# Kernel tuning notes

Measured on AMD Instinct MI355X. Metric: run time of the kernel, lower is better.

Reference implementation:

```python
import jax, jax.numpy as jnp
import numpy as np

N_HEADS = 8
N_POINTS = 4
EPS = 1e-5


def _conv1x1(x, w, b):
    # x: [B,C,H,W], w: [O,C]
    return jnp.einsum('bchw,oc->bohw', x, w) + b[None, :, None, None]


def _gn(x, g, b, groups=32):
    B, C, H, W = x.shape
    xr = x.reshape(B, groups, C // groups, H, W)
    m = xr.mean((2, 3, 4), keepdims=True)
    v = xr.var((2, 3, 4), keepdims=True)
    xn = ((xr - m) * jax.lax.rsqrt(v + EPS)).reshape(B, C, H, W)
    return xn * g[None, :, None, None] + b[None, :, None, None]


def _ln(x, g, b):
    m = x.mean(-1, keepdims=True)
    v = x.var(-1, keepdims=True)
    return (x - m) * jax.lax.rsqrt(v + EPS) * g + b


def _ln_spec(x, g2, b2, n):
    # modality-specific LayerNorm: separate params for v tokens [:n] and i tokens [n:]
    return jnp.concatenate([_ln(x[:, :n], g2[0], b2[0]), _ln(x[:, n:], g2[1], b2[1])], 1)


def _sine_pos(h, w, d):
    nf = d // 2
    scale = 2.0 * np.pi
    ye = jnp.arange(1, h + 1, dtype=jnp.float32) / h * scale
    xe = jnp.arange(1, w + 1, dtype=jnp.float32) / w * scale
    dim_t = 10000.0 ** (2.0 * (jnp.arange(nf) // 2).astype(jnp.float32) / nf)
    def enc(e):
        p = e[:, None] / dim_t
        return jnp.stack([jnp.sin(p[:, 0::2]), jnp.cos(p[:, 1::2])], -1).reshape(e.shape[0], nf)
    py = enc(ye)  # [h,nf]
    px = enc(xe)  # [w,nf]
    pos = jnp.concatenate([jnp.broadcast_to(py[:, None, :], (h, w, nf)),
                           jnp.broadcast_to(px[None, :, :], (h, w, nf))], -1)
    return pos.reshape(h * w, d)


def _bilinear(vl, loc):
    # vl: [B,h,w,Hd,Dh] value for one level, loc: [B,Lq,Hd,P,2] normalized (x,y)
    B, h, w, Hd, Dh = vl.shape
    Lq, P = loc.shape[1], loc.shape[3]
    x = loc[..., 0] * w - 0.5
    y = loc[..., 1] * h - 0.5
    x0 = jnp.floor(x)
    y0 = jnp.floor(y)
    wx = x - x0
    wy = y - y0
    x0i = x0.astype(jnp.int32)
    y0i = y0.astype(jnp.int32)
    v2 = vl.reshape(B, h * w, Hd, Dh).transpose(0, 2, 1, 3)  # [B,Hd,HW,Dh]
    def g(ix, iy):
        valid = ((ix >= 0) & (ix < w) & (iy >= 0) & (iy < h)).astype(vl.dtype)
        flat = jnp.clip(iy, 0, h - 1) * w + jnp.clip(ix, 0, w - 1)  # [B,Lq,Hd,P]
        idx = flat.transpose(0, 2, 1, 3).reshape(B, Hd, Lq * P)
        gv = jnp.take_along_axis(v2, idx[..., None], axis=2)  # [B,Hd,Lq*P,Dh]
        gv = gv.reshape(B, Hd, Lq, P, Dh).transpose(0, 2, 1, 3, 4)  # [B,Lq,Hd,P,Dh]
        return gv * valid[..., None]
    return (g(x0i, y0i) * ((1 - wx) * (1 - wy))[..., None]
            + g(x0i + 1, y0i) * (wx * (1 - wy))[..., None]
            + g(x0i, y0i + 1) * ((1 - wx) * wy)[..., None]
            + g(x0i + 1, y0i + 1) * (wx * wy)[..., None])


def _deform_attn(q, src, ref, shapes, ow, ob, aww, awb, vw, vb, opw, opb):
    B, Len, D = src.shape
    L = len(shapes)
    Hd, P = N_HEADS, N_POINTS
    Dh = D // Hd
    value = src @ vw + vb
    off = (q @ ow + ob).reshape(B, Len, Hd, L, P, 2)
    aw = jax.nn.softmax((q @ aww + awb).reshape(B, Len, Hd, L * P), -1).reshape(B, Len, Hd, L, P)
    norm = jnp.array([[s[1], s[0]] for s in shapes], jnp.float32)  # (w,h) per level
    loc = ref[None, :, None, None, None, :] + off / norm[None, None, None, :, None, :]
    out = jnp.zeros((B, Len, Hd, Dh), value.dtype)
    start = 0
    for l, (hh, ww) in enumerate(shapes):
        vl = value[:, start:start + hh * ww].reshape(B, hh, ww, Hd, Dh)
        samp = _bilinear(vl, loc[:, :, :, l])  # [B,Len,Hd,P,Dh]
        out = out + (samp * aw[:, :, :, l, :, None]).sum(3)
        start += hh * ww
    return out.reshape(B, Len, D) @ opw + opb


def _forward(input_v, input_i, av_w, av_b, av_g, av_be, ai_w, ai_b, ai_g, ai_be,
             level_embed, off_w, off_b, aw_w, aw_b, vp_w, vp_b, op_w, op_b,
             ln1_g, ln1_b, ffn1_w, ffn1_b, ffn2_w, ffn2_b, ln2_g, ln2_b,
             as_w, as_b, as_g, as_be):
    b, c, h, w = input_v.shape
    D = av_w.shape[0]
    hw = h * w
    fv = _gn(_conv1x1(input_v, av_w, av_b), av_g, av_be)
    fi = _gn(_conv1x1(input_i, ai_w, ai_b), ai_g, ai_be)
    sv = fv.reshape(b, D, hw).transpose(0, 2, 1)
    si = fi.reshape(b, D, hw).transpose(0, 2, 1)
    src = jnp.concatenate([sv, si], 1)  # [b, 2hw, D]
    pos = _sine_pos(h, w, D)
    posf = jnp.concatenate([pos + level_embed[0], pos + level_embed[1]], 0)
    gx = (jnp.arange(w, dtype=jnp.float32) + 0.5) / w
    gy = (jnp.arange(h, dtype=jnp.float32) + 0.5) / h
    X, Y = jnp.meshgrid(gx, gy)
    ref1 = jnp.stack([X, Y], -1).reshape(hw, 2)
    ref = jnp.concatenate([ref1, ref1], 0)  # [2hw, 2]
    shapes = [(h, w), (h, w)]
    for i in range(off_w.shape[0]):
        q = src + posf
        attn = _deform_attn(q, src, ref, shapes, off_w[i], off_b[i], aw_w[i], aw_b[i],
                            vp_w[i], vp_b[i], op_w[i], op_b[i])
        src = _ln_spec(src + attn, ln1_g[i], ln1_b[i], hw)
        ff = jax.nn.relu(src @ ffn1_w[i] + ffn1_b[i]) @ ffn2_w[i] + ffn2_b[i]
        src = _ln_spec(src + ff, ln2_g[i], ln2_b[i], hw)
    out = src[:, :hw] + src[:, hw:]  # chunk along tokens, sum modalities
    out = out.transpose(0, 2, 1).reshape(b, D, h, w)
    return _gn(_conv1x1(out, as_w, as_b), as_g, as_be)


def setup_inputs():
    key = jax.random.key(0)
    B, C, H, W = 16, 768, 20, 20
    D, NL, Hd, L, P, Dff = 512, 6, N_HEADS, 2, N_POINTS, 1024
    ks = iter(jax.random.split(key, 64))
    def rn(shape, scale=0.02):
        return jax.random.normal(next(ks), shape, jnp.float32) * scale
    return {
        'input_v': jax.random.normal(next(ks), (B, C, H, W), jnp.float32),
        'input_i': jax.random.normal(next(ks), (B, C, H, W), jnp.float32),
        'av_w': rn((D, C)), 'av_b': jnp.zeros((D,)), 'av_g': jnp.ones((D,)), 'av_be': jnp.zeros((D,)),
        'ai_w': rn((D, C)), 'ai_b': jnp.zeros((D,)), 'ai_g': jnp.ones((D,)), 'ai_be': jnp.zeros((D,)),
        'level_embed': rn((L, D)),
        'off_w': rn((NL, D, Hd * L * P * 2)), 'off_b': rn((NL, Hd * L * P * 2), 0.5),
        'aw_w': rn((NL, D, Hd * L * P)), 'aw_b': jnp.zeros((NL, Hd * L * P)),
        'vp_w': rn((NL, D, D)), 'vp_b': jnp.zeros((NL, D)),
        'op_w': rn((NL, D, D)), 'op_b': jnp.zeros((NL, D)),
        'ln1_g': jnp.ones((NL, 2, D)), 'ln1_b': jnp.zeros((NL, 2, D)),
        'ffn1_w': rn((NL, D, Dff)), 'ffn1_b': jnp.zeros((NL, Dff)),
        'ffn2_w': rn((NL, Dff, D)), 'ffn2_b': jnp.zeros((NL, D)),
        'ln2_g': jnp.ones((NL, 2, D)), 'ln2_b': jnp.zeros((NL, 2, D)),
        'as_w': rn((C, D)), 'as_b': jnp.zeros((C,)), 'as_g': jnp.ones((C,)), 'as_be': jnp.zeros((C,)),
    }


def reference(input_v, input_i, av_w, av_b, av_g, av_be, ai_w, ai_b, ai_g, ai_be,
              level_embed, off_w, off_b, aw_w, aw_b, vp_w, vp_b, op_w, op_b,
              ln1_g, ln1_b, ffn1_w, ffn1_b, ffn2_w, ffn2_b, ln2_g, ln2_b,
              as_w, as_b, as_g, as_be):
    return _forward(input_v, input_i, av_w, av_b, av_g, av_be, ai_w, ai_b, ai_g, ai_be,
                    level_embed, off_w, off_b, aw_w, aw_b, vp_w, vp_b, op_w, op_b,
                    ln1_g, ln1_b, ffn1_w, ffn1_b, ffn2_w, ffn2_b, ln2_g, ln2_b,
                    as_w, as_b, as_g, as_be)
```

## Files before the change

### kernel.cpp

```cpp
#include <hip/hip_runtime.h>
#include <hip/hip_bf16.h>
#include <cstddef>
#include <math.h>


constexpr int kB   = 16;
constexpr int kCin = 768;
constexpr int kHW  = 400;
constexpr int kWpx = 20;
constexpr int kHpx = 20;
constexpr int kD   = 512;
constexpr int kLen = 800;
constexpr int kDff = 1024;
constexpr int kNL  = 6;
constexpr float kEps = 1e-5f;

typedef __attribute__((ext_vector_type(8))) short s8v;
typedef __attribute__((ext_vector_type(4))) short s4v;
typedef __attribute__((ext_vector_type(4))) float f4v;

__device__ __forceinline__ int swzk(int row, int k) {
  return (k & ~31) | ((((k >> 3) + (row >> 1)) & 3) << 3) | (k & 7);
}

__device__ __forceinline__ unsigned short f2b(float f) {
  union { __hip_bfloat16 h; unsigned short u; } cv;
  cv.h = __float2bfloat16(f);
  return cv.u;
}

__device__ __forceinline__ float b2f(unsigned short u) {
  return __uint_as_float(((unsigned)u) << 16);
}

__device__ __forceinline__ void gll(const unsigned short* g, unsigned short* l) {
  __builtin_amdgcn_global_load_lds(
      (const __attribute__((address_space(1))) unsigned int*)g,
      (__attribute__((address_space(3))) unsigned int*)l, 16, 0, 0);
}

__device__ __forceinline__ void breduce2(float& s, float& s2, float* sh) {
#pragma unroll
  for (int o = 32; o > 0; o >>= 1) {
    s  += __shfl_down(s, o);
    s2 += __shfl_down(s2, o);
  }
  const int wid = threadIdx.x >> 6, lane = threadIdx.x & 63;
  if (lane == 0) { sh[wid] = s; sh[4 + wid] = s2; }
  __syncthreads();
  if (threadIdx.x == 0) {
    sh[0] = sh[0] + sh[1] + sh[2] + sh[3];
    sh[4] = sh[4] + sh[5] + sh[6] + sh[7];
  }
  __syncthreads();
  s = sh[0]; s2 = sh[4];
}

template<int EPI>
__global__ __launch_bounds__(256)
void mgemm(const unsigned short* __restrict__ Abf,
           const unsigned short* __restrict__ Bw,
           const float* __restrict__ bias,
           const unsigned short* __restrict__ resb,
           float* __restrict__ Cf, float* __restrict__ Cf2,
           const float* __restrict__ aux,
           unsigned short* __restrict__ Cb,
           int K, int ldc, int Nreal)
{
  __shared__ unsigned short As[2][4096];
  __shared__ unsigned short Bs[2][4096];
  const int tid = threadIdx.x;
  const int w = tid >> 6, l = tid & 63;
  const int m0 = blockIdx.y * 128;
  const int n0 = blockIdx.x * 128;

  f4v acc[4][4] = {};

  const int srow = w * 32 + (l >> 2);
  const unsigned short* ga0 = Abf + (size_t)(m0 + srow) * K + (l & 3) * 8;
  const unsigned short* ga1 = ga0 + (size_t)16 * K;
  const unsigned short* gb0 = Bw + (size_t)(n0 + srow) * K + (l & 3) * 8;
  const unsigned short* gb1 = gb0 + (size_t)16 * K;
  const int lb0 = (w * 32) * 32;
  const int lb1 = (w * 32 + 16) * 32;

  int aoff[4], boff[4];
#pragma unroll
  for (int f = 0; f < 4; f++) {
    const int ra = (w >> 1) * 64 + f * 16 + (l & 15);
    aoff[f] = ra * 32 + ((((l >> 4) + (ra >> 1)) & 3) << 3);
    const int rb = (w & 1) * 64 + f * 16 + (l & 15);
    boff[f] = rb * 32 + ((((l >> 4) + (rb >> 1)) & 3) << 3);
  }

  const int NT = K >> 5;
  gll(ga0, &As[0][lb0]); gll(ga1, &As[0][lb1]);
  gll(gb0, &Bs[0][lb0]); gll(gb1, &Bs[0][lb1]);
  __syncthreads();

  for (int t = 0; t < NT; ++t) {
    const int cur = t & 1;
    if (t + 1 < NT) {
      const int ko = (t + 1) * 32;
      const int nb = cur ^ 1;
      gll(ga0 + ko, &As[nb][lb0]); gll(ga1 + ko, &As[nb][lb1]);
      gll(gb0 + ko, &Bs[nb][lb0]); gll(gb1 + ko, &Bs[nb][lb1]);
    }
    s8v af[4], bf4[4];
#pragma unroll
    for (int f = 0; f < 4; f++) {
      af[f]  = *(const s8v*)&As[cur][aoff[f]];
      bf4[f] = *(const s8v*)&Bs[cur][boff[f]];
    }
#pragma unroll
    for (int i = 0; i < 4; i++)
#pragma unroll
      for (int j = 0; j < 4; j++)
        acc[i][j] = __builtin_amdgcn_mfma_f32_16x16x32_bf16(af[i], bf4[j], acc[i][j], 0, 0, 0);
    __syncthreads();
  }

  const int colb = n0 + (w & 1) * 64;
  const int rowb = m0 + (w >> 1) * 64 + (l >> 4) * 4;
#pragma unroll
  for (int i = 0; i < 4; i++) {
#pragma unroll
    for (int j = 0; j < 4; j++) {
      const int col = colb + j * 16 + (l & 15);
      float bv;
      if (EPI == 4) bv = (col < kD) ? bias[col] : 0.0f;
      else          bv = bias[col];
#pragma unroll
      for (int r = 0; r < 4; r++) {
        const int row = rowb + i * 16 + r;
        float v = acc[i][j][r] + bv;
        if (EPI == 0) {
          Cf[(size_t)row * ldc + col] = v;
        } else if (EPI == 1) {
          Cb[(size_t)row * ldc + swzk(row, col)] = f2b(fmaxf(v, 0.0f));
        } else if (EPI == 2) {
          v += b2f(resb[(size_t)row * kD + swzk(row, col)]);
          Cb[(size_t)row * kD + col] = f2b(v);
        } else if (EPI == 3) {
          const int bb = row / kHW, p = row % kHW;
          Cf[((size_t)bb * Nreal + col) * kHW + p] = v;
        } else if (EPI == 4) {
          if (col < kD) {
            Cb[(size_t)row * kD + col] = f2b(v);
          } else {
            const int c = col - kD;
            if (c < 192)
              Cf2[(size_t)row * 192 + c] = v + aux[(size_t)(row % kLen) * 192 + c];
          }
        } else {
          if (row < kLen) {
            const int ll = col >> 8, c = col & 255;
            if (c < 192)
              Cf[(((size_t)ll * kLen) + row) * 192 + c] = v;
          }
        }
      }
    }
  }
}

__device__ __forceinline__ void cvt8t(const float* __restrict__ W,
                                      unsigned short* __restrict__ out,
                                      int K, int N, int g)
{
  const int n = g % N;
  const int k = (g / N) * 8;
  s8v p;
#pragma unroll
  for (int j = 0; j < 8; j++) p[j] = (short)f2b(W[(size_t)(k + j) * N + n]);
  const int base = n * K + (k & ~31) + ((((k >> 3) + (n >> 1)) & 3) << 3);
  *(s8v*)&out[base] = p;
}

__global__ __launch_bounds__(256)
void cvt_all_k(const float* __restrict__ vp_w, const float* __restrict__ op_w,
               const float* __restrict__ off_w, const float* __restrict__ aw_w,
               const float* __restrict__ f1w_a, const float* __restrict__ f2w_a,
               unsigned short* __restrict__ wall)
{
  const int lyr = blockIdx.x / 832;
  int g = (blockIdx.x % 832) * 256 + threadIdx.x;
  unsigned short* wl = wall + (size_t)lyr * 1703936;
  if (g < 32768) { cvt8t(vp_w + (size_t)lyr * kD * kD, wl, 512, 512, g); return; }
  g -= 32768;
  if (g < 16384) {
    const int n = g & 255;
    const int k = (g >> 8) * 8;
    const float* ow  = off_w + (size_t)lyr * kD * 128;
    const float* aww = aw_w  + (size_t)lyr * kD * 64;
    s8v p;
#pragma unroll
    for (int j = 0; j < 8; j++) {
      float v = 0.0f;
      if (n < 128)      v = ow[(size_t)(k + j) * 128 + n];
      else if (n < 192) v = aww[(size_t)(k + j) * 64 + (n - 128)];
      p[j] = (short)f2b(v);
    }
    const int row = 512 + n;
    const int base = row * 512 + (k & ~31) + ((((k >> 3) + (row >> 1)) & 3) << 3);
    *(s8v*)&wl[base] = p;
    return;
  }
  g -= 16384;
  if (g < 32768) { cvt8t(op_w + (size_t)lyr * kD * kD, wl + 393216, 512, 512, g); return; }
  g -= 32768;
  if (g < 65536) { cvt8t(f1w_a + (size_t)lyr * kD * kDff, wl + 655360, 512, 1024, g); return; }
  g -= 65536;
  cvt8t(f2w_a + (size_t)lyr * kDff * kD, wl + 1179648, 1024, 512, g);
}

__global__ __launch_bounds__(256)
void cvt_pre_k(const float* __restrict__ off_w, const float* __restrict__ aw_w,
               const float* __restrict__ off_b, const float* __restrict__ aw_b,
               unsigned short* __restrict__ woaw_all, float* __restrict__ biasall)
{
  int g = blockIdx.x * 256 + threadIdx.x;
  if (g < 98304) {
    const int l = g >> 14;
    const int gg = g & 16383;
    const int n = gg & 255;
    const int k = (gg >> 8) * 8;
    const float* ow = off_w + (size_t)l * kD * 128;
    const float* aww = aw_w + (size_t)l * kD * 64;
    s8v p;
#pragma unroll
    for (int j = 0; j < 8; j++) {
      float v = 0.0f;
      if (n < 128)      v = ow[(size_t)(k + j) * 128 + n];
      else if (n < 192) v = aww[(size_t)(k + j) * 64 + (n - 128)];
      p[j] = (short)f2b(v);
    }
    const int row = l * 256 + n;
    const int base = row * 512 + (k & ~31) + ((((k >> 3) + (row >> 1)) & 3) << 3);
    *(s8v*)&woaw_all[base] = p;
    return;
  }
  g -= 98304;
  const int l = g >> 8, c = g & 255;
  float v = 0.0f;
  if (c < 128)      v = off_b[l * 128 + c];
  else if (c < 192) v = aw_b[l * 64 + (c - 128)];
  biasall[l * 256 + c] = v;
}

__global__ void cvtw_d_k(const float* __restrict__ W, unsigned short* __restrict__ out,
                         int K, int N)
{
  const int gid = blockIdx.x * 256 + threadIdx.x;
  const int K8 = K >> 3;
  const int n  = gid / K8;
  const int k  = (gid % K8) * 8;
  s8v p;
#pragma unroll
  for (int j = 0; j < 8; j++) p[j] = (short)f2b(W[(size_t)n * K + k + j]);
  const int base = n * K + (k & ~31) + ((((k >> 3) + (n >> 1)) & 3) << 3);
  *(s8v*)&out[base] = p;
}

__global__ void tin_k(const float* __restrict__ in, unsigned short* __restrict__ out)
{
  __shared__ float t[16][17];
  const int b = blockIdx.z, c0 = blockIdx.x * 16, p0 = blockIdx.y * 16;
  const int tx = threadIdx.x & 15, ty = threadIdx.x >> 4;
  t[ty][tx] = in[((size_t)b * kCin + c0 + ty) * kHW + p0 + tx];
  __syncthreads();
  const int row = b * kHW + p0 + ty;
  const int c = c0 + tx;
  out[(size_t)row * kCin + swzk(row, c)] = f2b(t[tx][ty]);
}

__global__ void posfb_k(unsigned short* __restrict__ posfb,
                        const float* __restrict__ level_embed)
{
  const int gid = blockIdx.x * 256 + threadIdx.x;
  const int d0 = (gid & 63) * 8;
  const int t  = gid >> 6;
  s8v o;
  if (t >= kLen) {
#pragma unroll
    for (int j = 0; j < 8; j++) o[j] = 0;
  } else {
    const int lvl = t / kHW;
    const int tt = t % kHW;
    const int yy = tt / kWpx, xx = tt % kWpx;
#pragma unroll
    for (int j = 0; j < 8; j++) {
      const int d = d0 + j;
      const int dd = d & 255;
      const float e = (d < 256) ? ((float)(yy + 1) * (6.283185307179586f / kHpx))
                                : ((float)(xx + 1) * (6.283185307179586f / kWpx));
      const float dimt = powf(10000.0f, (float)(dd >> 1) / 128.0f);
      const float pp = e / dimt;
      const float val = (dd & 1) ? cosf(pp) : sinf(pp);
      o[j] = (short)f2b(val + level_embed[lvl * kD + d]);
    }
  }
  *(s8v*)&posfb[(size_t)t * kD + swzk(t, d0)] = o;
}

__global__ __launch_bounds__(256)
void gn_stats_tok_k(const float* __restrict__ x, float* __restrict__ stats)
{
  __shared__ float sh[8];
  const int b = blockIdx.x >> 5;
  const int g = blockIdx.x & 31;
  const float* xb = x + (size_t)b * kHW * kD + g * 16;
  float s = 0.f, s2 = 0.f;
  for (int i = threadIdx.x; i < kHW * 16; i += 256) {
    const int p = i >> 4, j = i & 15;
    const float v = xb[(size_t)p * kD + j];
    s += v; s2 += v * v;
  }
  breduce2(s, s2, sh);
  if (threadIdx.x == 0) {
    const float mean = s / (kHW * 16.0f);
    const float var  = s2 / (kHW * 16.0f) - mean * mean;
    stats[blockIdx.x * 2]     = mean;
    stats[blockIdx.x * 2 + 1] = rsqrtf(var + kEps);
  }
}

__global__ void gn_norm_tok_k(const float* __restrict__ x,
                              unsigned short* __restrict__ srcb,
                              const float* __restrict__ stats,
                              const float* __restrict__ gam, const float* __restrict__ bet,
                              int tokoff)
{
  const int gid = blockIdx.x * 256 + threadIdx.x;
  const int d0 = (gid & 63) * 8;
  const int rest = gid >> 6;
  const int b = rest / kHW, p = rest % kHW;
  const int g = d0 >> 4;
  const float mean = stats[(b * 32 + g) * 2];
  const float rstd = stats[(b * 32 + g) * 2 + 1];
  const float* xr = x + ((size_t)(b * kHW + p)) * kD + d0;
  const int row = b * kLen + tokoff + p;
  s8v o;
#pragma unroll
  for (int j = 0; j < 8; j++)
    o[j] = (short)f2b((xr[j] - mean) * rstd * gam[d0 + j] + bet[d0 + j]);
  *(s8v*)&srcb[(size_t)row * kD + swzk(row, d0)] = o;
}

__global__ __launch_bounds__(256)
void gn_stats_ch_k(const float* __restrict__ x, float* __restrict__ stats)
{
  __shared__ float sh[8];
  const int b = blockIdx.x >> 5;
  const int g = blockIdx.x & 31;
  const float* xb = x + (size_t)b * kCin * kHW + (size_t)g * 24 * kHW;
  float s = 0.f, s2 = 0.f;
  for (int i = threadIdx.x; i < 24 * kHW; i += 256) {
    const float v = xb[i];
    s += v; s2 += v * v;
  }
  breduce2(s, s2, sh);
  if (threadIdx.x == 0) {
    const float mean = s / (24.0f * kHW);
    const float var  = s2 / (24.0f * kHW) - mean * mean;
    stats[blockIdx.x * 2]     = mean;
    stats[blockIdx.x * 2 + 1] = rsqrtf(var + kEps);
  }
}

__global__ void gn_norm_ch_k(const float* __restrict__ x, float* __restrict__ out,
                             const float* __restrict__ stats,
                             const float* __restrict__ gam, const float* __restrict__ bet)
{
  const int idx = blockIdx.x * 256 + threadIdx.x;
  const int rest = idx / kHW;
  const int c = rest % kCin;
  const int b = rest / kCin;
  const int g = c / 24;
  const float mean = stats[(b * 32 + g) * 2];
  const float rstd = stats[(b * 32 + g) * 2 + 1];
  out[idx] = (x[idx] - mean) * rstd * gam[c] + bet[c];
}

__global__ __launch_bounds__(256)
void ln4_k(const unsigned short* __restrict__ x, unsigned short* __restrict__ outb,
           const float* __restrict__ gamma, const float* __restrict__ beta)
{
  const int row = blockIdx.x * 4 + (threadIdx.x >> 6);
  const int l = threadIdx.x & 63;
  const int mod = ((row % kLen) < kHW) ? 0 : 1;
  const s8v u = *(const s8v*)&x[(size_t)row * kD + l * 8];
  float v[8];
#pragma unroll
  for (int j = 0; j < 8; j++) v[j] = b2f((unsigned short)u[j]);
  float s = 0.f, s2 = 0.f;
#pragma unroll
  for (int j = 0; j < 8; j++) { s += v[j]; s2 += v[j] * v[j]; }
#pragma unroll
  for (int o = 32; o > 0; o >>= 1) {
    s  += __shfl_xor(s, o);
    s2 += __shfl_xor(s2, o);
  }
  const float mean = s * (1.0f / kD);
  const float var  = s2 * (1.0f / kD) - mean * mean;
  const float rstd = rsqrtf(var + kEps);
  const float* g  = gamma + mod * kD + l * 8;
  const float* be = beta  + mod * kD + l * 8;
  s8v o8;
#pragma unroll
  for (int j = 0; j < 8; j++)
    o8[j] = (short)f2b((v[j] - mean) * rstd * g[j] + be[j]);
  *(s8v*)&outb[(size_t)row * kD + swzk(row, l * 8)] = o8;
}

__global__ __launch_bounds__(256)
void sample_k(const unsigned short* __restrict__ value, const float* __restrict__ offaw,
              unsigned short* __restrict__ out)
{
  __shared__ float wls[2][64][8];
  const int tid = threadIdx.x;
  const int tok = tid >> 7;
  const int wt  = tid & 127;
  const int token = blockIdx.x * 2 + tok;
  const int b = token / kLen;
  const int t = token % kLen;
  const int tt = t % kHW;

  if (wt < 64) {
    const int h = wt >> 3, lp = wt & 7, lvl = lp >> 2, p = lp & 3;
    const float* oa = offaw + (size_t)token * 192;
    const float lg = oa[128 + h * 8 + lp];
    float mx = lg;
#pragma unroll
    for (int msk = 1; msk < 8; msk <<= 1) mx = fmaxf(mx, __shfl_xor(mx, msk));
    const float ex = __expf(lg - mx);
    float ssum = ex;
#pragma unroll
    for (int msk = 1; msk < 8; msk <<= 1) ssum += __shfl_xor(ssum, msk);
    const float aw = ex / ssum;

    const float x = (float)(tt % kWpx) + oa[h * 16 + lvl * 8 + p * 2];
    const float y = (float)(tt / kWpx) + oa[h * 16 + lvl * 8 + p * 2 + 1];
    const float x0f = floorf(x), y0f = floorf(y);
    const float wx = x - x0f, wy = y - y0f;
    const int x0 = (int)x0f, y0 = (int)y0f;
    const int rowbase = b * kLen + lvl * kHW;
#pragma unroll
    for (int dy = 0; dy < 2; dy++) {
#pragma unroll
      for (int dx = 0; dx < 2; dx++) {
        const int ix = x0 + dx, iy = y0 + dy;
        const bool valid = (ix >= 0) & (ix < kWpx) & (iy >= 0) & (iy < kHpx);
        const float cw = (dx ? wx : 1.0f - wx) * (dy ? wy : 1.0f - wy);
        const float w = valid ? aw * cw : 0.0f;
        const int ixc = min(max(ix, 0), kWpx - 1);
        const int iyc = min(max(iy, 0), kHpx - 1);
        const int r = rowbase + iyc * kWpx + ixc;
        const int cn = dy * 2 + dx;
        wls[tok][wt][cn * 2]     = w;
        wls[tok][wt][cn * 2 + 1] = __int_as_float(r);
      }
    }
  }
  __syncthreads();

  const int c0 = wt * 4;
  const int h = wt >> 4;
  float acc0 = 0.f, acc1 = 0.f, acc2 = 0.f, acc3 = 0.f;
  const unsigned short* vb = value + c0;
#pragma unroll
  for (int pp = 0; pp < 8; pp++) {
    const float* wl = wls[tok][h * 8 + pp];
#pragma unroll
    for (int cn = 0; cn < 4; cn++) {
      const float w = wl[cn * 2];
      const int r = __float_as_int(wl[cn * 2 + 1]);
      const s4v q = *(const s4v*)(vb + (size_t)r * kD);
      acc0 += w * b2f((unsigned short)q[0]);
      acc1 += w * b2f((unsigned short)q[1]);
      acc2 += w * b2f((unsigned short)q[2]);
      acc3 += w * b2f((unsigned short)q[3]);
    }
  }
  const int sk = swzk(token, c0);
  s4v o;
  o[0] = (short)f2b(acc0); o[1] = (short)f2b(acc1);
  o[2] = (short)f2b(acc2); o[3] = (short)f2b(acc3);
  *(s4v*)&out[(size_t)token * kD + sk] = o;
}

__global__ void sumtok_k(const unsigned short* __restrict__ srcb,
                         unsigned short* __restrict__ tokb)
{
  const int gid = blockIdx.x * 256 + threadIdx.x;
  const int d0 = (gid & 63) * 8;
  const int rest = gid >> 6;
  const int b = rest / kHW, p = rest % kHW;
  const int r1 = b * kLen + p;
  const int r2 = r1 + kHW;
  const int ro = b * kHW + p;
  const s8v u1 = *(const s8v*)&srcb[(size_t)r1 * kD + swzk(r1, d0)];
  const s8v u2 = *(const s8v*)&srcb[(size_t)r2 * kD + swzk(r2, d0)];
  s8v o;
#pragma unroll
  for (int j = 0; j < 8; j++)
    o[j] = (short)f2b(b2f((unsigned short)u1[j]) + b2f((unsigned short)u2[j]));
  *(s8v*)&tokb[(size_t)ro * kD + swzk(ro, d0)] = o;
}

extern "C" void kernel_launch(void* const* d_in, const int* in_sizes, int n_in,
                              void* d_out, int out_size, void* d_ws, size_t ws_size,
                              hipStream_t stream)
{
  const float* input_v     = (const float*)d_in[0];
  const float* input_i     = (const float*)d_in[1];
  const float* av_w        = (const float*)d_in[2];
  const float* av_b        = (const float*)d_in[3];
  const float* av_g        = (const float*)d_in[4];
  const float* av_be       = (const float*)d_in[5];
  const float* ai_w        = (const float*)d_in[6];
  const float* ai_b        = (const float*)d_in[7];
  const float* ai_g        = (const float*)d_in[8];
  const float* ai_be       = (const float*)d_in[9];
  const float* level_embed = (const float*)d_in[10];
  const float* off_w       = (const float*)d_in[11];
  const float* off_b       = (const float*)d_in[12];
  const float* aw_w        = (const float*)d_in[13];
  const float* aw_b        = (const float*)d_in[14];
  const float* vp_w        = (const float*)d_in[15];
  const float* vp_b        = (const float*)d_in[16];
  const float* op_w        = (const float*)d_in[17];
  const float* op_b        = (const float*)d_in[18];
  const float* ln1_g       = (const float*)d_in[19];
  const float* ln1_b       = (const float*)d_in[20];
  const float* ffn1_w      = (const float*)d_in[21];
  const float* ffn1_b      = (const float*)d_in[22];
  const float* ffn2_w      = (const float*)d_in[23];
  const float* ffn2_b      = (const float*)d_in[24];
  const float* ln2_g       = (const float*)d_in[25];
  const float* ln2_b       = (const float*)d_in[26];
  const float* as_w        = (const float*)d_in[27];
  const float* as_b        = (const float*)d_in[28];
  const float* as_g        = (const float*)d_in[29];
  const float* as_be       = (const float*)d_in[30];

  float* wsf     = (float*)d_ws;
  float* offaw   = wsf;
  float* posWc   = offaw   + (size_t)2457600;
  float* biasall = posWc   + (size_t)921600;
  float* stats   = biasall + (size_t)1536;
  unsigned short* srcb     = (unsigned short*)(stats + 1024);
  unsigned short* bufA     = srcb     + (size_t)6553600;
  unsigned short* bufB     = bufA     + (size_t)13107200;
  unsigned short* wall     = bufB     + (size_t)6553600;
  unsigned short* wcs      = wall     + (size_t)10223616;
  unsigned short* woaw_all = wcs      + (size_t)393216;
  unsigned short* posfb    = woaw_all + (size_t)786432;
  float* wallf = (float*)wall;

  const int M  = kB * kLen;

  posfb_k<<<dim3(224), 256, 0, stream>>>(posfb, level_embed);
  cvt_pre_k<<<dim3(390), 256, 0, stream>>>(off_w, aw_w, off_b, aw_b,
                                           woaw_all, biasall);
  mgemm<5><<<dim3(12, 7), 256, 0, stream>>>(
      posfb, woaw_all, biasall, nullptr, posWc, nullptr, nullptr, nullptr,
      512, 0, 0);

  for (int mod = 0; mod < 2; mod++) {
    const float* in  = mod ? input_i : input_v;
    const float* cw  = mod ? ai_w  : av_w;
    const float* cb  = mod ? ai_b  : av_b;
    const float* cg  = mod ? ai_g  : av_g;
    const float* cbe = mod ? ai_be : av_be;
    tin_k<<<dim3(48, 25, 16), 256, 0, stream>>>(in, bufA);
    cvtw_d_k<<<dim3(192), 256, 0, stream>>>(cw, wcs, 768, 512);
    mgemm<0><<<dim3(4, 50), 256, 0, stream>>>(
        bufA, wcs, cb, nullptr, wallf, nullptr, nullptr, nullptr, 768, 512, 0);
    gn_stats_tok_k<<<dim3(kB * 32), 256, 0, stream>>>(wallf, stats);
    gn_norm_tok_k<<<dim3(1600), 256, 0, stream>>>(
        wallf, srcb, stats, cg, cbe, mod * kHW);
  }

  cvt_all_k<<<dim3(4992), 256, 0, stream>>>(vp_w, op_w, off_w, aw_w,
                                            ffn1_w, ffn2_w, wall);

  for (int l = 0; l < kNL; l++) {
    unsigned short* wcomb = wall + (size_t)l * 1703936;
    unsigned short* wop   = wcomb + 393216;
    unsigned short* wf1   = wcomb + 655360;
    unsigned short* wf2   = wcomb + 1179648;
    const float* vbl  = vp_b   + (size_t)l * kD;
    const float* opbl = op_b   + (size_t)l * kD;
    const float* l1g  = ln1_g  + (size_t)l * 2 * kD;
    const float* l1b  = ln1_b  + (size_t)l * 2 * kD;
    const float* f1b  = ffn1_b + (size_t)l * kDff;
    const float* f2b_ = ffn2_b + (size_t)l * kD;
    const float* l2g  = ln2_g  + (size_t)l * 2 * kD;
    const float* l2b  = ln2_b  + (size_t)l * 2 * kD;

    mgemm<4><<<dim3(6, 100), 256, 0, stream>>>(
        srcb, wcomb, vbl, nullptr, nullptr, offaw, posWc + (size_t)l * 153600,
        bufA, 512, 0, 0);

    sample_k<<<dim3(M / 2), 256, 0, stream>>>(bufA, offaw, bufB);

    mgemm<2><<<dim3(4, 100), 256, 0, stream>>>(
        bufB, wop, opbl, srcb, nullptr, nullptr, nullptr, bufA, 512, 512, 0);

    ln4_k<<<dim3(M / 4), 256, 0, stream>>>(bufA, srcb, l1g, l1b);

    mgemm<1><<<dim3(8, 100), 256, 0, stream>>>(
        srcb, wf1, f1b, nullptr, nullptr, nullptr, nullptr, bufA, 512, 1024, 0);
    mgemm<2><<<dim3(4, 100), 256, 0, stream>>>(
        bufA, wf2, f2b_, srcb, nullptr, nullptr, nullptr, bufB, 1024, 512, 0);

    ln4_k<<<dim3(M / 4), 256, 0, stream>>>(bufB, srcb, l2g, l2b);
  }

  sumtok_k<<<dim3(1600), 256, 0, stream>>>(srcb, bufA);
  cvtw_d_k<<<dim3(192), 256, 0, stream>>>(as_w, wcs, 512, 768);
  mgemm<3><<<dim3(6, 50), 256, 0, stream>>>(
      bufA, wcs, as_b, nullptr, wallf, nullptr, nullptr, nullptr, 512, 0, 768);
  gn_stats_ch_k<<<dim3(kB * 32), 256, 0, stream>>>(wallf, stats);
  gn_norm_ch_k<<<dim3(19200), 256, 0, stream>>>(
      wallf, (float*)d_out, stats, as_g, as_be);
}
```

Before: 1.117 ms.

## Triple-buffer GEMM loads and batch both modality input projections

The shared GEMM kernel moves from double to triple buffering in LDS. It prefetches two k-tiles ahead and uses explicit vmcnt waits with a single barrier per iteration, which should hide more global-load latency. The two per-modality input-projection pipelines (transpose, weight convert, GEMM, GN stats, GN norm) are merged into one launch each, with the GEMM choosing weights per M-half. The GEMM output is stored as bf16 instead of fp32 before group norm. This gives fewer launches and less traffic, but the triple buffers use more LDS, which may lower occupancy, and the bf16 intermediate adds rounding before the GN statistics.

New measurement: 1.098 ms. No clear change (-1.7%).

```diff
diff --git a/kernel.cpp b/kernel.cpp
--- a/kernel.cpp
+++ b/kernel.cpp
@@ -67,12 +67,14 @@
            unsigned short* __restrict__ Cb,
            int K, int ldc, int Nreal)
 {
-  __shared__ unsigned short As[2][4096];
-  __shared__ unsigned short Bs[2][4096];
+  __shared__ unsigned short As[3][4096];
+  __shared__ unsigned short Bs[3][4096];
   const int tid = threadIdx.x;
   const int w = tid >> 6, l = tid & 63;
   const int m0 = blockIdx.y * 128;
   const int n0 = blockIdx.x * 128;
+
+  if (EPI == 6 && m0 >= 6400) { Bw = resb; bias = aux; }
 
   f4v acc[4][4] = {};
 
@@ -93,19 +95,23 @@
     boff[f] = rb * 32 + ((((l >> 4) + (rb >> 1)) & 3) << 3);
   }
 
+#define STAGE(ko, bi) do { \
+    gll(ga0 + (ko), &As[bi][lb0]); gll(ga1 + (ko), &As[bi][lb1]); \
+    gll(gb0 + (ko), &Bs[bi][lb0]); gll(gb1 + (ko), &Bs[bi][lb1]); } while (0)
+
   const int NT = K >> 5;
-  gll(ga0, &As[0][lb0]); gll(ga1, &As[0][lb1]);
-  gll(gb0, &Bs[0][lb0]); gll(gb1, &Bs[0][lb1]);
-  __syncthreads();
-
+  STAGE(0, 0);
+  STAGE(32, 1);
+
+  int cur = 0;
+  int bpre = 2;
+  int kpre = 64;
   for (int t = 0; t < NT; ++t) {
-    const int cur = t & 1;
-    if (t + 1 < NT) {
-      const int ko = (t + 1) * 32;
-      const int nb = cur ^ 1;
-      gll(ga0 + ko, &As[nb][lb0]); gll(ga1 + ko, &As[nb][lb1]);
-      gll(gb0 + ko, &Bs[nb][lb0]); gll(gb1 + ko, &Bs[nb][lb1]);
-    }
+    if (t + 1 < NT) asm volatile("s_waitcnt vmcnt(4)" ::: "memory");
+    else            asm volatile("s_waitcnt vmcnt(0)" ::: "memory");
+    __builtin_amdgcn_s_barrier();
+    __builtin_amdgcn_sched_barrier(0);
+    if (t + 2 < NT) STAGE(kpre, bpre);
     s8v af[4], bf4[4];
 #pragma unroll
     for (int f = 0; f < 4; f++) {
@@ -117,8 +123,11 @@
 #pragma unroll
       for (int j = 0; j < 4; j++)
         acc[i][j] = __builtin_amdgcn_mfma_f32_16x16x32_bf16(af[i], bf4[j], acc[i][j], 0, 0, 0);
-    __syncthreads();
-  }
+    kpre += 32;
+    bpre = (bpre == 2) ? 0 : bpre + 1;
+    cur  = (cur == 2) ? 0 : cur + 1;
+  }
+#undef STAGE
 
   const int colb = n0 + (w & 1) * 64;
   const int rowb = m0 + (w >> 1) * 64 + (l >> 4) * 4;
@@ -134,9 +143,7 @@
       for (int r = 0; r < 4; r++) {
         const int row = rowb + i * 16 + r;
         float v = acc[i][j][r] + bv;
-        if (EPI == 0) {
-          Cf[(size_t)row * ldc + col] = v;
-        } else if (EPI == 1) {
+        if (EPI == 1) {
           Cb[(size_t)row * ldc + swzk(row, col)] = f2b(fmaxf(v, 0.0f));
         } else if (EPI == 2) {
           v += b2f(resb[(size_t)row * kD + swzk(row, col)]);
@@ -152,12 +159,14 @@
             if (c < 192)
               Cf2[(size_t)row * 192 + c] = v + aux[(size_t)(row % kLen) * 192 + c];
           }
-        } else {
+        } else if (EPI == 5) {
           if (row < kLen) {
             const int ll = col >> 8, c = col & 255;
             if (c < 192)
               Cf[(((size_t)ll * kLen) + row) * 192 + c] = v;
           }
+        } else {
+          Cb[(size_t)row * kD + col] = f2b(v);
         }
       }
     }
@@ -262,14 +271,34 @@
   *(s8v*)&out[base] = p;
 }
 
-__global__ void tin_k(const float* __restrict__ in, unsigned short* __restrict__ out)
+__global__ void cvtw_dd_k(const float* __restrict__ W0, const float* __restrict__ W1,
+                          unsigned short* __restrict__ out)
+{
+  int gid = blockIdx.x * 256 + threadIdx.x;
+  const float* W = W0;
+  unsigned short* o = out;
+  if (gid >= 49152) { gid -= 49152; W = W1; o = out + 393216; }
+  const int n = gid / 96;
+  const int k = (gid % 96) * 8;
+  s8v p;
+#pragma unroll
+  for (int j = 0; j < 8; j++) p[j] = (short)f2b(W[(size_t)n * kCin + k + j]);
+  const int base = n * kCin + (k & ~31) + ((((k >> 3) + (n >> 1)) & 3) << 3);
+  *(s8v*)&o[base] = p;
+}
+
+__global__ void tin_k(const float* __restrict__ inv, const float* __restrict__ ini,
+                      unsigned short* __restrict__ out)
 {
   __shared__ float t[16][17];
-  const int b = blockIdx.z, c0 = blockIdx.x * 16, p0 = blockIdx.y * 16;
+  const int z = blockIdx.z;
+  const int mod = z >> 4, b = z & 15;
+  const float* in = (mod ? ini : inv) + (size_t)b * kCin * kHW;
+  const int c0 = blockIdx.x * 16, p0 = blockIdx.y * 16;
   const int tx = threadIdx.x & 15, ty = threadIdx.x >> 4;
-  t[ty][tx] = in[((size_t)b * kCin + c0 + ty) * kHW + p0 + tx];
+  t[ty][tx] = in[((size_t)(c0 + ty)) * kHW + p0 + tx];
   __syncthreads();
-  const int row = b * kHW + p0 + ty;
+  const int row = z * kHW + p0 + ty;
   const int c = c0 + tx;
   out[(size_t)row * kCin + swzk(row, c)] = f2b(t[tx][ty]);
 }
@@ -304,17 +333,21 @@
 }
 
 __global__ __launch_bounds__(256)
-void gn_stats_tok_k(const float* __restrict__ x, float* __restrict__ stats)
+void gn_stats_tok_k(const unsigned short* __restrict__ x, float* __restrict__ stats)
 {
   __shared__ float sh[8];
-  const int b = blockIdx.x >> 5;
+  const int mb = blockIdx.x >> 5;
   const int g = blockIdx.x & 31;
-  const float* xb = x + (size_t)b * kHW * kD + g * 16;
+  const unsigned short* xb = x + (size_t)mb * kHW * kD + g * 16;
   float s = 0.f, s2 = 0.f;
-  for (int i = threadIdx.x; i < kHW * 16; i += 256) {
-    const int p = i >> 4, j = i & 15;
-    const float v = xb[(size_t)p * kD + j];
-    s += v; s2 += v * v;
+  for (int i = threadIdx.x; i < 800; i += 256) {
+    const int p = i >> 1, half = i & 1;
+    const s8v u = *(const s8v*)&xb[(size_t)p * kD + half * 8];
+#pragma unroll
+    for (int j = 0; j < 8; j++) {
+      const float v = b2f((unsigned short)u[j]);
+      s += v; s2 += v * v;
+    }
   }
   breduce2(s, s2, sh);
   if (threadIdx.x == 0) {
@@ -325,25 +358,29 @@
   }
 }
 
-__global__ void gn_norm_tok_k(const float* __restrict__ x,
+__global__ void gn_norm_tok_k(const unsigned short* __restrict__ x,
                               unsigned short* __restrict__ srcb,
                               const float* __restrict__ stats,
-                              const float* __restrict__ gam, const float* __restrict__ bet,
-                              int tokoff)
+                              const float* __restrict__ gv, const float* __restrict__ bev,
+                              const float* __restrict__ gi, const float* __restrict__ bei)
 {
   const int gid = blockIdx.x * 256 + threadIdx.x;
   const int d0 = (gid & 63) * 8;
-  const int rest = gid >> 6;
-  const int b = rest / kHW, p = rest % kHW;
+  const int rl = gid >> 6;
+  const int mb = rl / kHW;
+  const int p  = rl - mb * kHW;
+  const int mod = mb >> 4, b = mb & 15;
   const int g = d0 >> 4;
-  const float mean = stats[(b * 32 + g) * 2];
-  const float rstd = stats[(b * 32 + g) * 2 + 1];
-  const float* xr = x + ((size_t)(b * kHW + p)) * kD + d0;
-  const int row = b * kLen + tokoff + p;
+  const float mean = stats[(mb * 32 + g) * 2];
+  const float rstd = stats[(mb * 32 + g) * 2 + 1];
+  const float* gam = mod ? gi : gv;
+  const float* bet = mod ? bei : bev;
+  const s8v u = *(const s8v*)&x[(size_t)rl * kD + d0];
+  const int row = b * kLen + mod * kHW + p;
   s8v o;
 #pragma unroll
   for (int j = 0; j < 8; j++)
-    o[j] = (short)f2b((xr[j] - mean) * rstd * gam[d0 + j] + bet[d0 + j]);
+    o[j] = (short)f2b((b2f((unsigned short)u[j]) - mean) * rstd * gam[d0 + j] + bet[d0 + j]);
   *(s8v*)&srcb[(size_t)row * kD + swzk(row, d0)] = o;
 }
 
@@ -549,16 +586,16 @@
   float* posWc   = offaw   + (size_t)2457600;
   float* biasall = posWc   + (size_t)921600;
   float* stats   = biasall + (size_t)1536;
-  unsigned short* srcb     = (unsigned short*)(stats + 1024);
+  unsigned short* srcb     = (unsigned short*)(stats + 2048);
   unsigned short* bufA     = srcb     + (size_t)6553600;
   unsigned short* bufB     = bufA     + (size_t)13107200;
   unsigned short* wall     = bufB     + (size_t)6553600;
   unsigned short* wcs      = wall     + (size_t)10223616;
-  unsigned short* woaw_all = wcs      + (size_t)393216;
+  unsigned short* woaw_all = wcs      + (size_t)786432;
   unsigned short* posfb    = woaw_all + (size_t)786432;
   float* wallf = (float*)wall;
 
-  const int M  = kB * kLen;
+  const int M = kB * kLen;
 
   posfb_k<<<dim3(224), 256, 0, stream>>>(posfb, level_embed);
   cvt_pre_k<<<dim3(390), 256, 0, stream>>>(off_w, aw_w, off_b, aw_b,
@@ -567,20 +604,13 @@
       posfb, woaw_all, biasall, nullptr, posWc, nullptr, nullptr, nullptr,
       512, 0, 0);
 
-  for (int mod = 0; mod < 2; mod++) {
-    const float* in  = mod ? input_i : input_v;
-    const float* cw  = mod ? ai_w  : av_w;
-    const float* cb  = mod ? ai_b  : av_b;
-    const float* cg  = mod ? ai_g  : av_g;
-    const float* cbe = mod ? ai_be : av_be;
-    tin_k<<<dim3(48, 25, 16), 256, 0, stream>>>(in, bufA);
-    cvtw_d_k<<<dim3(192), 256, 0, stream>>>(cw, wcs, 768, 512);
-    mgemm<0><<<dim3(4, 50), 256, 0, stream>>>(
-        bufA, wcs, cb, nullptr, wallf, nullptr, nullptr, nullptr, 768, 512, 0);
-    gn_stats_tok_k<<<dim3(kB * 32), 256, 0, stream>>>(wallf, stats);
-    gn_norm_tok_k<<<dim3(1600), 256, 0, stream>>>(
-        wallf, srcb, stats, cg, cbe, mod * kHW);
-  }
+  tin_k<<<dim3(48, 25, 32), 256, 0, stream>>>(input_v, input_i, bufA);
+  cvtw_dd_k<<<dim3(384), 256, 0, stream>>>(av_w, ai_w, wcs);
+  mgemm<6><<<dim3(4, 100), 256, 0, stream>>>(
+      bufA, wcs, av_b, wcs + 393216, nullptr, nullptr, ai_b, bufB, 768, 512, 0);
+  gn_stats_tok_k<<<dim3(1024), 256, 0, stream>>>(bufB, stats);
+  gn_norm_tok_k<<<dim3(3200), 256, 0, stream>>>(
+      bufB, srcb, stats, av_g, av_be, ai_g, ai_be);
 
   cvt_all_k<<<dim3(4992), 256, 0, stream>>>(vp_w, op_w, off_w, aw_w,
                                             ffn1_w, ffn2_w, wall);
```
